# Kernel tuning notes

Hardware: AMD Instinct MI355X
Metric: run time of the kernel (lower is better)

## Reference

```python
import jax, jax.numpy as jnp
import numpy as np


def setup_inputs() -> dict:
    key = jax.random.key(0)
    k1, k2, k3, k4 = jax.random.split(key, 4)
    B, S, D_IN, D_OUT = 4, 2048, 1024, 1024
    x = jax.random.normal(k1, (B, S, D_IN), dtype=jnp.float32)
    # torch Linear weights: shape [d_out, d_in], scaled like kaiming-uniform-ish init
    scale = 1.0 / np.sqrt(D_IN)
    Wq = jax.random.normal(k2, (D_OUT, D_IN), dtype=jnp.float32) * scale
    Wk = jax.random.normal(k3, (D_OUT, D_IN), dtype=jnp.float32) * scale
    Wv = jax.random.normal(k4, (D_OUT, D_IN), dtype=jnp.float32) * scale
    return {"x": x, "Wq": Wq, "Wk": Wk, "Wv": Wv}


def reference(x, Wq, Wk, Wv):
    # x: [B, S, d_in]; W*: [d_out, d_in] (torch Linear convention y = x @ W.T)
    q = jnp.einsum("bsd,od->bso", x, Wq)
    k = jnp.einsum("bsd,od->bso", x, Wk)
    v = jnp.einsum("bsd,od->bso", x, Wv)
    d_out = k.shape[-1]
    scores = jnp.einsum("bqo,bko->bqk", q, k)  # [B, S, S]
    S = scores.shape[-1]
    causal = jnp.tril(jnp.ones((S, S), dtype=bool))  # True where allowed
    scores = jnp.where(causal, scores, -jnp.inf)
    weights = jax.nn.softmax(scores / jnp.sqrt(jnp.float32(d_out)), axis=-1)
    return jnp.einsum("bqk,bko->bqo", weights, v)
```

## Files before the change

kernel.cpp:

```cpp
#include <hip/hip_runtime.h>
#include <hip/hip_bf16.h>
#include <stdint.h>

typedef short bf16x8 __attribute__((ext_vector_type(8)));
typedef float f32x4 __attribute__((ext_vector_type(4)));

__device__ __forceinline__ float b2f(unsigned short u) {
    union { unsigned int i; float f; } c; c.i = ((unsigned int)u) << 16; return c.f;
}
__device__ __forceinline__ unsigned short f2b(float f) {
    union { float f; unsigned int i; } c; c.f = f;
    unsigned int u = c.i;
    u += 0x7fffu + ((u >> 16) & 1u);
    return (unsigned short)(u >> 16);
}

__device__ __forceinline__ void gload_lds16(const void* g, void* l) {
    __builtin_amdgcn_global_load_lds(
        (const __attribute__((address_space(1))) void*)g,
        (__attribute__((address_space(3))) void*)l, 16, 0, 0);
}

__global__ __launch_bounds__(256) void convert_all(const float* __restrict__ x,
                                                   const float* __restrict__ Wq,
                                                   const float* __restrict__ Wk,
                                                   const float* __restrict__ Wv,
                                                   unsigned short* __restrict__ xb,
                                                   unsigned short* __restrict__ wb) {
    const long X4 = 2097152, W4 = 262144, TOT = X4 + 3 * W4;
    long i = (long)blockIdx.x * blockDim.x + threadIdx.x;
    long stride = (long)gridDim.x * blockDim.x;
    for (; i < TOT; i += stride) {
        const float4* src;
        ushort4* dst;
        if (i < X4) {
            src = (const float4*)x + i;
            dst = (ushort4*)xb + i;
        } else {
            long j = i - X4;
            int w = (int)(j >> 18);
            long off = j & (W4 - 1);
            const float* s = (w == 0) ? Wq : (w == 1) ? Wk : Wv;
            src = (const float4*)s + off;
            dst = (ushort4*)wb + (long)w * W4 + off;
        }
        float4 v = *src;
        ushort4 o;
        o.x = f2b(v.x); o.y = f2b(v.y); o.z = f2b(v.z); o.w = f2b(v.w);
        *dst = o;
    }
}

__global__ __launch_bounds__(256) void transpose_bf16(const unsigned short* __restrict__ in,
                                                      unsigned short* __restrict__ out,
                                                      int S, int D) {
    __shared__ unsigned short tile[64][65];
    int d0 = blockIdx.x * 64, s0 = blockIdx.y * 64;
    long base = (long)blockIdx.z * S * D;
    int t = threadIdx.x;
    #pragma unroll
    for (int it = 0; it < 4; it++) {
        int u = it * 256 + t;
        int r = u >> 4, c4 = (u & 15) * 4;
        ushort4 v = *(const ushort4*)&in[base + (long)(s0 + r) * D + d0 + c4];
        tile[r][c4 + 0] = v.x; tile[r][c4 + 1] = v.y;
        tile[r][c4 + 2] = v.z; tile[r][c4 + 3] = v.w;
    }
    __syncthreads();
    #pragma unroll
    for (int it = 0; it < 4; it++) {
        int u = it * 256 + t;
        int rr = u >> 4, c4 = (u & 15) * 4;
        ushort4 o;
        o.x = tile[c4 + 0][rr]; o.y = tile[c4 + 1][rr];
        o.z = tile[c4 + 2][rr]; o.w = tile[c4 + 3][rr];
        *(ushort4*)&out[base + (long)(d0 + rr) * S + s0 + c4] = o;
    }
}

__global__ __launch_bounds__(256) void row_linv(const float* __restrict__ lp,
                                                float* __restrict__ linv) {
    int r = blockIdx.x * 256 + threadIdx.x;
    int q = r & 2047;
    int ns = ((q >> 7) + 1) * 2;
    float s = 0.f;
    for (int i = 0; i < ns; i++) s += lp[i * 8192 + r];
    linv[r] = 1.f / s;
}

#define BM 128
#define BN 128
#define BK 64

template <int MODE>
__global__ __launch_bounds__(256)
void gemm_bt(const unsigned short* __restrict__ A, const unsigned short* __restrict__ B,
             void* __restrict__ C0, void* __restrict__ C1, void* __restrict__ C2,
             int M, int N, int K,
             long sA, long sB, long sC, int lda, int ldb, int ldc) {
    int mb, nb;
    if (MODE == 1) {
        int l = blockIdx.x;
        mb = (int)((sqrtf(8.f * l + 1.f) - 1.f) * 0.5f);
        while ((mb + 1) * (mb + 2) / 2 <= l) mb++;
        while (mb * (mb + 1) / 2 > l) mb--;
        nb = l - mb * (mb + 1) / 2;
    } else if (MODE == 2) {
        mb = gridDim.y - 1 - blockIdx.y;
        nb = blockIdx.x;
    } else {
        mb = blockIdx.y;
        nb = blockIdx.x;
    }
    int bz = blockIdx.z;

    __shared__ unsigned short As[BM * BK];
    __shared__ unsigned short Bs[BN * BK];

    const unsigned short* Ab = A + (long)bz * sA;
    const unsigned short* Bb = B + (long)bz * sB;

    const int t = threadIdx.x;
    const int lane = t & 63;
    const int wid = t >> 6;
    const int wr = wid >> 1, wc = wid & 1;
    const int m0 = mb * BM, n0 = nb * BN;

    int Keff = K;
    if (MODE == 2) Keff = min(K, m0 + BM);

    f32x4 acc[4][4];
    #pragma unroll
    for (int i = 0; i < 4; i++)
        #pragma unroll
        for (int j = 0; j < 4; j++) acc[i][j] = (f32x4){0.f, 0.f, 0.f, 0.f};

    int rowS[4], csrc[4];
    #pragma unroll
    for (int i = 0; i < 4; i++) {
        int u = i * 256 + t;
        rowS[i] = u >> 3;
        csrc[i] = (u & 7) ^ (rowS[i] & 7);
    }

    for (int k0 = 0; k0 < Keff; k0 += BK) {
        __syncthreads();
        #pragma unroll
        for (int i = 0; i < 4; i++) {
            const unsigned short* gp = Ab + (long)(m0 + rowS[i]) * lda + k0 + csrc[i] * 8;
            gload_lds16(gp, (void*)&As[(i * 256 + wid * 64) * 8]);
        }
        #pragma unroll
        for (int i = 0; i < 4; i++) {
            const unsigned short* gp = Bb + (long)(n0 + rowS[i]) * ldb + k0 + csrc[i] * 8;
            gload_lds16(gp, (void*)&Bs[(i * 256 + wid * 64) * 8]);
        }
        asm volatile("s_waitcnt vmcnt(0)" ::: "memory");
        __syncthreads();

        #pragma unroll
        for (int s = 0; s < 2; s++) {
            bf16x8 af[4], bfr[4];
            int kc = s * 4 + (lane >> 4);
            #pragma unroll
            for (int m = 0; m < 4; m++) {
                int r = wr * 64 + m * 16 + (lane & 15);
                int c = kc ^ (r & 7);
                af[m] = *(const bf16x8*)&As[r * BK + c * 8];
            }
            #pragma unroll
            for (int n = 0; n < 4; n++) {
                int r = wc * 64 + n * 16 + (lane & 15);
                int c = kc ^ (r & 7);
                bfr[n] = *(const bf16x8*)&Bs[r * BK + c * 8];
            }
            #pragma unroll
            for (int m = 0; m < 4; m++)
                #pragma unroll
                for (int n = 0; n < 4; n++)
                    acc[m][n] = __builtin_amdgcn_mfma_f32_16x16x32_bf16(af[m], bfr[n], acc[m][n], 0, 0, 0);
        }
    }

    const int r0 = (lane >> 4) * 4;
    const int cf = lane & 15;
    if (MODE == 0) {
        int buf = n0 >> 10;
        unsigned short* Cb = (unsigned short*)(buf == 0 ? C0 : (buf == 1 ? C1 : C2));
        float scale = (buf == 0) ? 0.03125f : 1.0f;
        #pragma unroll
        for (int m = 0; m < 4; m++)
            #pragma unroll
            for (int n = 0; n < 4; n++)
                #pragma unroll
                for (int r = 0; r < 4; r++) {
                    long grow = m0 + wr * 64 + m * 16 + r0 + r;
                    int gcol = (n0 & 1023) + wc * 64 + n * 16 + cf;
                    Cb[grow * 1024 + gcol] = f2b(acc[m][n][r] * scale);
                }
    } else if (MODE == 1) {
        unsigned short* Cb = (unsigned short*)C0 + (long)bz * sC;
        float* lp = (float*)C1;
        float srow[4][4];
        #pragma unroll
        for (int m = 0; m < 4; m++)
            #pragma unroll
            for (int r = 0; r < 4; r++) srow[m][r] = 0.f;
        #pragma unroll
        for (int m = 0; m < 4; m++)
            #pragma unroll
            for (int n = 0; n < 4; n++)
                #pragma unroll
                for (int r = 0; r < 4; r++) {
                    int grow = m0 + wr * 64 + m * 16 + r0 + r;
                    int gcol = n0 + wc * 64 + n * 16 + cf;
                    float e = (gcol <= grow) ? __expf(acc[m][n][r]) : 0.f;
                    srow[m][r] += e;
                    Cb[(long)grow * ldc + gcol] = f2b(e);
                }
        #pragma unroll
        for (int m = 0; m < 4; m++)
            #pragma unroll
            for (int r = 0; r < 4; r++) {
                float s = srow[m][r];
                s += __shfl_xor(s, 1);
                s += __shfl_xor(s, 2);
                s += __shfl_xor(s, 4);
                s += __shfl_xor(s, 8);
                if ((lane & 15) == 0) {
                    int grow = m0 + wr * 64 + m * 16 + r0 + r;
                    lp[(nb * 2 + wc) * 8192 + bz * 2048 + grow] = s;
                }
            }
    } else {
        float* Cb = (float*)C0 + (long)bz * sC;
        const float* linv = (const float*)C1;
        #pragma unroll
        for (int m = 0; m < 4; m++)
            #pragma unroll
            for (int r = 0; r < 4; r++) {
                long grow = m0 + wr * 64 + m * 16 + r0 + r;
                float sc = linv[bz * 2048 + grow];
                #pragma unroll
                for (int n = 0; n < 4; n++) {
                    int gcol = n0 + wc * 64 + n * 16 + cf;
                    Cb[grow * ldc + gcol] = acc[m][n][r] * sc;
                }
            }
    }
}

extern "C" void kernel_launch(void* const* d_in, const int* in_sizes, int n_in,
                              void* d_out, int out_size, void* d_ws, size_t ws_size,
                              hipStream_t stream) {
    const float* x  = (const float*)d_in[0];
    const float* Wq = (const float*)d_in[1];
    const float* Wk = (const float*)d_in[2];
    const float* Wv = (const float*)d_in[3];

    char* ws = (char*)d_ws;
    unsigned short* xb = (unsigned short*)(ws);
    unsigned short* wb = (unsigned short*)(ws + 16777216);
    unsigned short* Qb = (unsigned short*)(ws + 23068672);
    unsigned short* Kb = (unsigned short*)(ws + 39845888);
    unsigned short* Vb = (unsigned short*)(ws + 56623104);
    unsigned short* Vt = (unsigned short*)(ws + 73400320);
    unsigned short* Sb = (unsigned short*)(ws + 90177536);
    float* lp   = (float*)(ws);
    float* linv = (float*)(ws + 1048576);

    convert_all<<<dim3(2048), dim3(256), 0, stream>>>(x, Wq, Wk, Wv, xb, wb);

    gemm_bt<0><<<dim3(24, 64, 1), 256, 0, stream>>>(
        xb, wb, Qb, Kb, Vb, 8192, 3072, 1024, 0L, 0L, 0L, 1024, 1024, 1024);

    transpose_bf16<<<dim3(16, 32, 4), 256, 0, stream>>>(Vb, Vt, 2048, 1024);

    gemm_bt<1><<<dim3(136, 1, 4), 256, 0, stream>>>(
        Qb, Kb, Sb, lp, nullptr, 2048, 2048, 1024,
        2048L * 1024, 2048L * 1024, 2048L * 2048, 1024, 1024, 2048);

    row_linv<<<dim3(32), dim3(256), 0, stream>>>(lp, linv);

    gemm_bt<2><<<dim3(8, 16, 4), 256, 0, stream>>>(
        Sb, Vt, d_out, linv, nullptr, 2048, 1024, 2048,
        2048L * 2048, 1024L * 2048, 2048L * 1024, 2048, 2048, 1024);
}
```

Before: 178.4 us.

## Fuse V transpose into QKV projection epilogue via LDS staging

Removes the separate transpose_bf16 kernel. The QKV GEMM now writes V directly in transposed layout: each wave stages its tile through swizzled LDS and then issues vectorized 16-byte stores into Vt. This drops one kernel launch and the extra write and read of V through global memory. It also changes the MODE 2 block ordering so that batches alternate between reverse and forward row order, presumably to balance causal work across the grid.

```diff
diff --git a/kernel.cpp b/kernel.cpp
--- a/kernel.cpp
+++ b/kernel.cpp
@@ -51,33 +51,6 @@
     }
 }
 
-__global__ __launch_bounds__(256) void transpose_bf16(const unsigned short* __restrict__ in,
-                                                      unsigned short* __restrict__ out,
-                                                      int S, int D) {
-    __shared__ unsigned short tile[64][65];
-    int d0 = blockIdx.x * 64, s0 = blockIdx.y * 64;
-    long base = (long)blockIdx.z * S * D;
-    int t = threadIdx.x;
-    #pragma unroll
-    for (int it = 0; it < 4; it++) {
-        int u = it * 256 + t;
-        int r = u >> 4, c4 = (u & 15) * 4;
-        ushort4 v = *(const ushort4*)&in[base + (long)(s0 + r) * D + d0 + c4];
-        tile[r][c4 + 0] = v.x; tile[r][c4 + 1] = v.y;
-        tile[r][c4 + 2] = v.z; tile[r][c4 + 3] = v.w;
-    }
-    __syncthreads();
-    #pragma unroll
-    for (int it = 0; it < 4; it++) {
-        int u = it * 256 + t;
-        int rr = u >> 4, c4 = (u & 15) * 4;
-        ushort4 o;
-        o.x = tile[c4 + 0][rr]; o.y = tile[c4 + 1][rr];
-        o.z = tile[c4 + 2][rr]; o.w = tile[c4 + 3][rr];
-        *(ushort4*)&out[base + (long)(d0 + rr) * S + s0 + c4] = o;
-    }
-}
-
 __global__ __launch_bounds__(256) void row_linv(const float* __restrict__ lp,
                                                 float* __restrict__ linv) {
     int r = blockIdx.x * 256 + threadIdx.x;
@@ -106,7 +79,7 @@
         while (mb * (mb + 1) / 2 > l) mb--;
         nb = l - mb * (mb + 1) / 2;
     } else if (MODE == 2) {
-        mb = gridDim.y - 1 - blockIdx.y;
+        mb = (blockIdx.z & 2) ? (gridDim.y - 1 - blockIdx.y) : blockIdx.y;
         nb = blockIdx.x;
     } else {
         mb = blockIdx.y;
@@ -114,8 +87,8 @@
     }
     int bz = blockIdx.z;
 
-    __shared__ unsigned short As[BM * BK];
-    __shared__ unsigned short Bs[BN * BK];
+    __shared__ unsigned short As[BM * BK + BN * BK];
+    unsigned short* Bs = As + BM * BK;
 
     const unsigned short* Ab = A + (long)bz * sA;
     const unsigned short* Bb = B + (long)bz * sB;
@@ -186,18 +159,50 @@
     const int cf = lane & 15;
     if (MODE == 0) {
         int buf = n0 >> 10;
-        unsigned short* Cb = (unsigned short*)(buf == 0 ? C0 : (buf == 1 ? C1 : C2));
-        float scale = (buf == 0) ? 0.03125f : 1.0f;
-        #pragma unroll
-        for (int m = 0; m < 4; m++)
-            #pragma unroll
-            for (int n = 0; n < 4; n++)
-                #pragma unroll
-                for (int r = 0; r < 4; r++) {
-                    long grow = m0 + wr * 64 + m * 16 + r0 + r;
-                    int gcol = (n0 & 1023) + wc * 64 + n * 16 + cf;
-                    Cb[grow * 1024 + gcol] = f2b(acc[m][n][r] * scale);
-                }
+        if (buf < 2) {
+            unsigned short* Cb = (unsigned short*)(buf == 0 ? C0 : C1);
+            float scale = (buf == 0) ? 0.03125f : 1.0f;
+            #pragma unroll
+            for (int m = 0; m < 4; m++)
+                #pragma unroll
+                for (int n = 0; n < 4; n++)
+                    #pragma unroll
+                    for (int r = 0; r < 4; r++) {
+                        long grow = m0 + wr * 64 + m * 16 + r0 + r;
+                        int gcol = (n0 & 1023) + wc * 64 + n * 16 + cf;
+                        Cb[grow * 1024 + gcol] = f2b(acc[m][n][r] * scale);
+                    }
+        } else {
+            __syncthreads();
+            unsigned short* tw = As + wid * 4096;
+            #pragma unroll
+            for (int m = 0; m < 4; m++)
+                #pragma unroll
+                for (int n = 0; n < 4; n++) {
+                    int dl = n * 16 + cf;
+                    int swz = (dl & 7) << 3;
+                    #pragma unroll
+                    for (int rp = 0; rp < 2; rp++) {
+                        int sl = m * 16 + r0 + rp * 2;
+                        unsigned int pk = (unsigned int)f2b(acc[m][n][rp * 2]) |
+                                          ((unsigned int)f2b(acc[m][n][rp * 2 + 1]) << 16);
+                        *(unsigned int*)&tw[dl * 64 + (sl ^ swz)] = pk;
+                    }
+                }
+            unsigned short* Vt = (unsigned short*)C2;
+            long vbase = ((long)(m0 >> 11) * 1024 + (n0 & 1023) + wc * 64) * 2048
+                         + (m0 & 2047) + wr * 64;
+            #pragma unroll
+            for (int pass = 0; pass < 4; pass++) {
+                int rr = (lane >> 2) + pass * 16;
+                int c8 = (lane & 3) * 16;
+                int swz = (rr & 7) << 3;
+                bf16x8 v0 = *(const bf16x8*)&tw[rr * 64 + (c8 ^ swz)];
+                bf16x8 v1 = *(const bf16x8*)&tw[rr * 64 + ((c8 + 8) ^ swz)];
+                *(bf16x8*)&Vt[vbase + (long)rr * 2048 + c8] = v0;
+                *(bf16x8*)&Vt[vbase + (long)rr * 2048 + c8 + 8] = v1;
+            }
+        }
     } else if (MODE == 1) {
         unsigned short* Cb = (unsigned short*)C0 + (long)bz * sC;
         float* lp = (float*)C1;
@@ -263,7 +268,6 @@
     unsigned short* wb = (unsigned short*)(ws + 16777216);
     unsigned short* Qb = (unsigned short*)(ws + 23068672);
     unsigned short* Kb = (unsigned short*)(ws + 39845888);
-    unsigned short* Vb = (unsigned short*)(ws + 56623104);
     unsigned short* Vt = (unsigned short*)(ws + 73400320);
     unsigned short* Sb = (unsigned short*)(ws + 90177536);
     float* lp   = (float*)(ws);
@@ -272,9 +276,7 @@
     convert_all<<<dim3(2048), dim3(256), 0, stream>>>(x, Wq, Wk, Wv, xb, wb);
 
     gemm_bt<0><<<dim3(24, 64, 1), 256, 0, stream>>>(
-        xb, wb, Qb, Kb, Vb, 8192, 3072, 1024, 0L, 0L, 0L, 1024, 1024, 1024);
-
-    transpose_bf16<<<dim3(16, 32, 4), 256, 0, stream>>>(Vb, Vt, 2048, 1024);
+        xb, wb, Qb, Kb, Vt, 8192, 3072, 1024, 0L, 0L, 0L, 1024, 1024, 1024);
 
     gemm_bt<1><<<dim3(136, 1, 4), 256, 0, stream>>>(
         Qb, Kb, Sb, lp, nullptr, 2048, 2048, 1024,
```

Measured after the change: 172.8 us. 1.03x faster.
